# Kernel optimization log

Measured on AMD Instinct MI355X. Metric: run time of the kernel, lower is better.

## Reference

```python
import jax, jax.numpy as jnp
import numpy as np

B, N, IN_F, OUT_F = 32, 1024, 256, 256
ALPHA = 0.2  # LeakyReLU negative slope
NEG_INF = -9e15  # matches torch's -9000000000000000.0 masking constant


def setup_inputs() -> dict:
    key = jax.random.key(0)
    k1, k2, k3, k4 = jax.random.split(key, 4)
    h = jax.random.normal(k1, (B, N, IN_F), dtype=jnp.float32)
    adj = jax.random.randint(k2, (B, N, N), 0, 2, dtype=jnp.int32)
    W = jax.random.normal(k3, (OUT_F, IN_F), dtype=jnp.float32) * 0.05
    a = jax.random.normal(k4, (1, 2 * OUT_F), dtype=jnp.float32) * 0.05
    return {"h": h, "adj": adj, "W": W, "a": a}


def reference(h, adj, W, a):
    # Wh: (B, N, out)
    Wh = jnp.einsum("bni,oi->bno", h, W)
    # Decompose a([Wh_i || Wh_j]) = Wh_i . a1 + Wh_j . a2 (identical math,
    # avoids the O(B*N^2*2*out) concat intermediate of the torch code).
    a1 = a[0, :OUT_F]   # (out,)
    a2 = a[0, OUT_F:]   # (out,)
    si = Wh @ a1        # (B, N) score contribution of source node i
    sj = Wh @ a2        # (B, N) score contribution of neighbor node j
    e = jax.nn.leaky_relu(si[:, :, None] + sj[:, None, :], negative_slope=ALPHA)
    attention = jnp.where(adj > 0, e, NEG_INF)
    attention = jax.nn.softmax(attention, axis=-1)
    # dropout omitted (eval mode)
    h_prime = jnp.einsum("bij,bjo->bio", attention, Wh)
    return jax.nn.elu(h_prime)
```

## Files before the change

kernel.cpp:

```cpp
#include <hip/hip_runtime.h>
#include <hip/hip_bf16.h>


#define ALPHA 0.2f
#define LOG2E 1.44269504f

typedef __bf16 bf16x8 __attribute__((ext_vector_type(8)));
typedef __bf16 bf16x4 __attribute__((ext_vector_type(4)));
typedef float  f32x4  __attribute__((ext_vector_type(4)));
typedef unsigned long long u64;

__global__ __launch_bounds__(256) void k1_gemm1(const float* __restrict__ h,
                                                const float* __restrict__ W,
                                                const float* __restrict__ a_g,
                                                __bf16* __restrict__ whT,
                                                float* __restrict__ si,
                                                float* __restrict__ sj) {
    __shared__ __bf16 hA[64 * 72];
    __shared__ __bf16 hB[256 * 72];
    __shared__ float  red[512];
    const int t    = threadIdx.x;
    const int r0   = blockIdx.x * 64;
    const int b    = r0 >> 10;
    const int n0   = r0 & 1023;
    const int w    = t >> 6;
    const int l    = t & 63;
    const int ln   = l & 15;
    const int quad = l >> 4;

    f32x4 acc[4][4] = {};
    float4 ha_r[4], wb_r[16];

    #pragma unroll
    for (int it = 0; it < 4; ++it)
        ha_r[it] = *(const float4*)&h[(size_t)(r0 + it * 16 + (t >> 4)) * 256 + (t & 15) * 4];
    #pragma unroll
    for (int it = 0; it < 16; ++it)
        wb_r[it] = *(const float4*)&W[(size_t)(it * 16 + (t >> 4)) * 256 + (t & 15) * 4];

    for (int kc = 0; kc < 4; ++kc) {
        #pragma unroll
        for (int it = 0; it < 4; ++it) {
            const float4 v = ha_r[it];
            bf16x4 pv = {(__bf16)v.x, (__bf16)v.y, (__bf16)v.z, (__bf16)v.w};
            *(bf16x4*)&hA[(it * 16 + (t >> 4)) * 72 + (t & 15) * 4] = pv;
        }
        #pragma unroll
        for (int it = 0; it < 16; ++it) {
            const float4 v = wb_r[it];
            bf16x4 pv = {(__bf16)v.x, (__bf16)v.y, (__bf16)v.z, (__bf16)v.w};
            *(bf16x4*)&hB[(it * 16 + (t >> 4)) * 72 + (t & 15) * 4] = pv;
        }
        __syncthreads();
        if (kc < 3) {
            const int k0 = (kc + 1) * 64;
            #pragma unroll
            for (int it = 0; it < 4; ++it)
                ha_r[it] = *(const float4*)&h[(size_t)(r0 + it * 16 + (t >> 4)) * 256 + k0 + (t & 15) * 4];
            #pragma unroll
            for (int it = 0; it < 16; ++it)
                wb_r[it] = *(const float4*)&W[(size_t)(it * 16 + (t >> 4)) * 256 + k0 + (t & 15) * 4];
        }
        #pragma unroll
        for (int kk = 0; kk < 2; ++kk) {
            bf16x8 af[4], bfr[4];
            #pragma unroll
            for (int ri = 0; ri < 4; ++ri)
                af[ri] = *(const bf16x8*)&hA[(ri * 16 + ln) * 72 + kk * 32 + quad * 8];
            #pragma unroll
            for (int oi = 0; oi < 4; ++oi)
                bfr[oi] = *(const bf16x8*)&hB[(w * 64 + oi * 16 + ln) * 72 + kk * 32 + quad * 8];
            #pragma unroll
            for (int ri = 0; ri < 4; ++ri)
                #pragma unroll
                for (int oi = 0; oi < 4; ++oi)
                    acc[ri][oi] = __builtin_amdgcn_mfma_f32_16x16x32_bf16(
                        af[ri], bfr[oi], acc[ri][oi], 0, 0, 0);
        }
        __syncthreads();
    }

    #pragma unroll
    for (int ri = 0; ri < 4; ++ri) {
        const int n = ri * 16 + quad * 4;
        #pragma unroll
        for (int oi = 0; oi < 4; ++oi) {
            const int o = w * 64 + oi * 16 + ln;
            bf16x4 pv = {(__bf16)acc[ri][oi][0], (__bf16)acc[ri][oi][1],
                         (__bf16)acc[ri][oi][2], (__bf16)acc[ri][oi][3]};
            *(bf16x4*)&hB[o * 72 + n] = pv;
        }
    }
    __syncthreads();

    #pragma unroll
    for (int it = 0; it < 8; ++it) {
        const int o   = w * 64 + it * 8 + (l >> 3);
        const int seg = l & 7;
        const bf16x8 v = *(const bf16x8*)&hB[o * 72 + seg * 8];
        *(bf16x8*)&whT[((size_t)b * 256 + o) * 1024 + n0 + seg * 8] = v;
    }

    {
        float s1 = 0.f, s2 = 0.f;
        #pragma unroll 8
        for (int oi = 0; oi < 64; ++oi) {
            const int o = w * 64 + oi;
            const float v = (float)hB[o * 72 + l];
            s1 += v * a_g[o];
            s2 += v * a_g[256 + o];
        }
        red[w * 64 + l]       = s1;
        red[256 + w * 64 + l] = s2;
    }
    __syncthreads();
    if (t < 64) {
        si[b * 1024 + n0 + t] =
            (red[t] + red[64 + t] + red[128 + t] + red[192 + t]) * LOG2E;
    } else if (t < 128) {
        const int n = t - 64;
        sj[b * 1024 + n0 + n] =
            (red[256 + n] + red[320 + n] + red[384 + n] + red[448 + n]) * LOG2E;
    }
}

__global__ __launch_bounds__(256) void k3_attn(const int* __restrict__ adj,
                                               const __bf16* __restrict__ whT,
                                               const float* __restrict__ si_g,
                                               const float* __restrict__ sj_g,
                                               float* __restrict__ out) {
    __shared__ __bf16 lds_s[2][64 * 72];
    __shared__ float  lds_denom[64];
    const int t = threadIdx.x;
    const int orig = blockIdx.x;
    const int wgid = (orig & 7) * 64 + (orig >> 3);
    const int b    = wgid >> 4;
    const int i0   = (wgid & 15) << 6;
    const int w    = t >> 6;
    const int l    = t & 63;
    const int ln   = l & 15;
    const int quad = l >> 4;
    const int g    = t >> 4;
    const int j4   = t & 15;

    float si_r[4];
    #pragma unroll
    for (int m = 0; m < 4; ++m) si_r[m] = si_g[b * 1024 + i0 + m * 16 + g];

    float dsum[4] = {0.f, 0.f, 0.f, 0.f};
    f32x4 acc[4][4] = {};
    const __bf16* whTb = whT + (size_t)b * 256 * 1024;
    const int*    adjb = adj + ((size_t)(b * 1024 + i0)) * 1024;

    int4   amsk[4];
    float4 sjv;
    #pragma unroll
    for (int m = 0; m < 4; ++m)
        amsk[m] = *(const int4*)&adjb[(size_t)(m * 16 + g) * 1024 + j4 * 4];
    sjv = *(const float4*)&sj_g[b * 1024 + j4 * 4];

    #pragma unroll 2
    for (int jc = 0; jc < 16; ++jc) {
        const int j0 = jc * 64;
        __bf16* s_buf = (__bf16*)lds_s[jc & 1];

        bf16x8 bfr[2][4];
        #pragma unroll
        for (int kk = 0; kk < 2; ++kk)
            #pragma unroll
            for (int oi = 0; oi < 4; ++oi)
                bfr[kk][oi] = *(const bf16x8*)&whTb[
                    (size_t)(w * 64 + oi * 16 + ln) * 1024 + j0 + kk * 32 + quad * 8];

        #pragma unroll
        for (int m = 0; m < 4; ++m) {
            const int il = m * 16 + g;
            float e0 = si_r[m] + sjv.x; e0 = e0 > 0.f ? e0 : ALPHA * e0;
            float e1 = si_r[m] + sjv.y; e1 = e1 > 0.f ? e1 : ALPHA * e1;
            float e2 = si_r[m] + sjv.z; e2 = e2 > 0.f ? e2 : ALPHA * e2;
            float e3 = si_r[m] + sjv.w; e3 = e3 > 0.f ? e3 : ALPHA * e3;
            const float w0 = amsk[m].x > 0 ? exp2f(e0) : 0.f;
            const float w1 = amsk[m].y > 0 ? exp2f(e1) : 0.f;
            const float w2 = amsk[m].z > 0 ? exp2f(e2) : 0.f;
            const float w3 = amsk[m].w > 0 ? exp2f(e3) : 0.f;
            bf16x4 pv = {(__bf16)w0, (__bf16)w1, (__bf16)w2, (__bf16)w3};
            dsum[m] += (float)pv[0] + (float)pv[1] + (float)pv[2] + (float)pv[3];
            *(bf16x4*)&s_buf[il * 72 + j4 * 4] = pv;
        }

        if (jc < 15) {
            #pragma unroll
            for (int m = 0; m < 4; ++m)
                amsk[m] = *(const int4*)&adjb[(size_t)(m * 16 + g) * 1024 + j0 + 64 + j4 * 4];
            sjv = *(const float4*)&sj_g[b * 1024 + j0 + 64 + j4 * 4];
        }
        __syncthreads();

        #pragma unroll
        for (int kk = 0; kk < 2; ++kk) {
            bf16x8 af[4];
            #pragma unroll
            for (int ri = 0; ri < 4; ++ri)
                af[ri] = *(const bf16x8*)&s_buf[(ri * 16 + ln) * 72 + kk * 32 + quad * 8];
            #pragma unroll
            for (int ri = 0; ri < 4; ++ri)
                #pragma unroll
                for (int oi = 0; oi < 4; ++oi)
                    acc[ri][oi] = __builtin_amdgcn_mfma_f32_16x16x32_bf16(
                        af[ri], bfr[kk][oi], acc[ri][oi], 0, 0, 0);
        }
    }

    #pragma unroll
    for (int m = 0; m < 4; ++m) {
        float v = dsum[m];
        v += __shfl_xor(v, 1);
        v += __shfl_xor(v, 2);
        v += __shfl_xor(v, 4);
        v += __shfl_xor(v, 8);
        if (j4 == 0) lds_denom[m * 16 + g] = v;
    }
    __syncthreads();
    #pragma unroll
    for (int ri = 0; ri < 4; ++ri) {
        #pragma unroll
        for (int q = 0; q < 4; ++q) {
            const int il = ri * 16 + quad * 4 + q;
            const float dinv = 1.0f / fmaxf(lds_denom[il], 1e-30f);
            #pragma unroll
            for (int oi = 0; oi < 4; ++oi) {
                const int o = w * 64 + oi * 16 + ln;
                const float v = acc[ri][oi][q] * dinv;
                const float r = v > 0.f ? v : __expf(v) - 1.f;
                out[((size_t)(b * 1024 + i0 + il)) * 256 + o] = r;
            }
        }
    }
}

extern "C" void kernel_launch(void* const* d_in, const int* in_sizes, int n_in,
                              void* d_out, int out_size, void* d_ws, size_t ws_size,
                              hipStream_t stream) {
    const float* h   = (const float*)d_in[0];
    const int*   adj = (const int*)d_in[1];
    const float* W   = (const float*)d_in[2];
    const float* a   = (const float*)d_in[3];
    float* out = (float*)d_out;

    __bf16* whT = (__bf16*)d_ws;
    float*  si  = (float*)((char*)d_ws + (size_t)16777216);
    float*  sj  = (float*)((char*)d_ws + (size_t)16777216 + 131072);

    k1_gemm1<<<512, 256, 0, stream>>>(h, W, a, whT, si, sj);
    k3_attn<<<512, 256, 0, stream>>>(adj, whT, si, sj, out);
}
```

Before: 257.4 us.

## Halve attention tile rows, double grid, and explicitly double-buffer mask loads

Shrinks the attention kernel's row tile from 64 to 32 rows per block, doubling the grid to 1024 blocks, and sets launch bounds to request 4 blocks per SM for higher occupancy. The main loop is manually unrolled by two with ping-pong register buffers for the adjacency and sj prefetch, which are now issued earlier, before the exp computation. The intent is more waves to hide the latency of the adj stream and WhT loads. In exchange, each block re-reads the full WhT B operand, so that traffic doubles, and each MFMA B fragment is reused over fewer rows.

```diff
diff --git a/kernel.cpp b/kernel.cpp
--- a/kernel.cpp
+++ b/kernel.cpp
@@ -124,18 +124,72 @@
     }
 }
 
-__global__ __launch_bounds__(256) void k3_attn(const int* __restrict__ adj,
-                                               const __bf16* __restrict__ whT,
-                                               const float* __restrict__ si_g,
-                                               const float* __restrict__ sj_g,
-                                               float* __restrict__ out) {
-    __shared__ __bf16 lds_s[2][64 * 72];
-    __shared__ float  lds_denom[64];
+#define K3_BODY(JC, ACUR, SJCUR, ANXT, SJNXT, SBUF)                                    \
+  {                                                                                    \
+    const int j0 = (JC) * 64;                                                          \
+             \
+    bf16x8 bfr[2][4];                                                                  \
+    _Pragma("unroll")                                                                  \
+    for (int kk = 0; kk < 2; ++kk)                                                     \
+      _Pragma("unroll")                                                                \
+      for (int oi = 0; oi < 4; ++oi)                                                   \
+        bfr[kk][oi] = *(const bf16x8*)&whTb[                                           \
+            (size_t)(w * 64 + oi * 16 + ln) * 1024 + j0 + kk * 32 + quad * 8];         \
+            \
+    if ((JC) < 15) {                                                                   \
+      _Pragma("unroll")                                                                \
+      for (int m = 0; m < 2; ++m)                                                      \
+        ANXT[m] = *(const int4*)&adjb[(size_t)(m * 16 + g) * 1024 + j0 + 64 + j4 * 4]; \
+      SJNXT = *(const float4*)&sj_g[b * 1024 + j0 + 64 + j4 * 4];                      \
+    }                                                                                  \
+                \
+    _Pragma("unroll")                                                                  \
+    for (int m = 0; m < 2; ++m) {                                                      \
+      const int il = m * 16 + g;                                                       \
+      float e0 = si_r[m] + SJCUR.x; e0 = e0 > 0.f ? e0 : ALPHA * e0;                   \
+      float e1 = si_r[m] + SJCUR.y; e1 = e1 > 0.f ? e1 : ALPHA * e1;                   \
+      float e2 = si_r[m] + SJCUR.z; e2 = e2 > 0.f ? e2 : ALPHA * e2;                   \
+      float e3 = si_r[m] + SJCUR.w; e3 = e3 > 0.f ? e3 : ALPHA * e3;                   \
+      const float w0 = ACUR[m].x > 0 ? exp2f(e0) : 0.f;                                \
+      const float w1 = ACUR[m].y > 0 ? exp2f(e1) : 0.f;                                \
+      const float w2 = ACUR[m].z > 0 ? exp2f(e2) : 0.f;                                \
+      const float w3 = ACUR[m].w > 0 ? exp2f(e3) : 0.f;                                \
+      bf16x4 pv = {(__bf16)w0, (__bf16)w1, (__bf16)w2, (__bf16)w3};                    \
+      dsum[m] += (float)pv[0] + (float)pv[1] + (float)pv[2] + (float)pv[3];            \
+      *(bf16x4*)&SBUF[il * 72 + j4 * 4] = pv;                                          \
+    }                                                                                  \
+    __syncthreads();                                                                   \
+                         \
+    _Pragma("unroll")                                                                  \
+    for (int kk = 0; kk < 2; ++kk) {                                                   \
+      bf16x8 af[2];                                                                    \
+      _Pragma("unroll")                                                                \
+      for (int ri = 0; ri < 2; ++ri)                                                   \
+        af[ri] = *(const bf16x8*)&SBUF[(ri * 16 + ln) * 72 + kk * 32 + quad * 8];      \
+      _Pragma("unroll")                                                                \
+      for (int ri = 0; ri < 2; ++ri)                                                   \
+        _Pragma("unroll")                                                              \
+        for (int oi = 0; oi < 4; ++oi)                                                 \
+          acc[ri][oi] = __builtin_amdgcn_mfma_f32_16x16x32_bf16(                       \
+              af[ri], bfr[kk][oi], acc[ri][oi], 0, 0, 0);                              \
+    }                                                                                  \
+             \
+                                   \
+  }
+
+__global__ __launch_bounds__(256, 4) void k3_attn(const int* __restrict__ adj,
+                                                  const __bf16* __restrict__ whT,
+                                                  const float* __restrict__ si_g,
+                                                  const float* __restrict__ sj_g,
+                                                  float* __restrict__ out) {
+    __shared__ __bf16 lds_s0[32 * 72];
+    __shared__ __bf16 lds_s1[32 * 72];
+    __shared__ float  lds_denom[32];
     const int t = threadIdx.x;
     const int orig = blockIdx.x;
-    const int wgid = (orig & 7) * 64 + (orig >> 3);
-    const int b    = wgid >> 4;
-    const int i0   = (wgid & 15) << 6;
+    const int wgid = (orig & 7) * 128 + (orig >> 3);
+    const int b    = wgid >> 5;
+    const int i0   = (wgid & 31) << 5;
     const int w    = t >> 6;
     const int l    = t & 63;
     const int ln   = l & 15;
@@ -143,76 +197,29 @@
     const int g    = t >> 4;
     const int j4   = t & 15;
 
-    float si_r[4];
-    #pragma unroll
-    for (int m = 0; m < 4; ++m) si_r[m] = si_g[b * 1024 + i0 + m * 16 + g];
-
-    float dsum[4] = {0.f, 0.f, 0.f, 0.f};
-    f32x4 acc[4][4] = {};
+    float si_r[2];
+    #pragma unroll
+    for (int m = 0; m < 2; ++m) si_r[m] = si_g[b * 1024 + i0 + m * 16 + g];
+
+    float dsum[2] = {0.f, 0.f};
+    f32x4 acc[2][4] = {};
     const __bf16* whTb = whT + (size_t)b * 256 * 1024;
     const int*    adjb = adj + ((size_t)(b * 1024 + i0)) * 1024;
 
-    int4   amsk[4];
-    float4 sjv;
-    #pragma unroll
-    for (int m = 0; m < 4; ++m)
-        amsk[m] = *(const int4*)&adjb[(size_t)(m * 16 + g) * 1024 + j4 * 4];
-    sjv = *(const float4*)&sj_g[b * 1024 + j4 * 4];
-
-    #pragma unroll 2
-    for (int jc = 0; jc < 16; ++jc) {
-        const int j0 = jc * 64;
-        __bf16* s_buf = (__bf16*)lds_s[jc & 1];
-
-        bf16x8 bfr[2][4];
-        #pragma unroll
-        for (int kk = 0; kk < 2; ++kk)
-            #pragma unroll
-            for (int oi = 0; oi < 4; ++oi)
-                bfr[kk][oi] = *(const bf16x8*)&whTb[
-                    (size_t)(w * 64 + oi * 16 + ln) * 1024 + j0 + kk * 32 + quad * 8];
-
-        #pragma unroll
-        for (int m = 0; m < 4; ++m) {
-            const int il = m * 16 + g;
-            float e0 = si_r[m] + sjv.x; e0 = e0 > 0.f ? e0 : ALPHA * e0;
-            float e1 = si_r[m] + sjv.y; e1 = e1 > 0.f ? e1 : ALPHA * e1;
-            float e2 = si_r[m] + sjv.z; e2 = e2 > 0.f ? e2 : ALPHA * e2;
-            float e3 = si_r[m] + sjv.w; e3 = e3 > 0.f ? e3 : ALPHA * e3;
-            const float w0 = amsk[m].x > 0 ? exp2f(e0) : 0.f;
-            const float w1 = amsk[m].y > 0 ? exp2f(e1) : 0.f;
-            const float w2 = amsk[m].z > 0 ? exp2f(e2) : 0.f;
-            const float w3 = amsk[m].w > 0 ? exp2f(e3) : 0.f;
-            bf16x4 pv = {(__bf16)w0, (__bf16)w1, (__bf16)w2, (__bf16)w3};
-            dsum[m] += (float)pv[0] + (float)pv[1] + (float)pv[2] + (float)pv[3];
-            *(bf16x4*)&s_buf[il * 72 + j4 * 4] = pv;
-        }
-
-        if (jc < 15) {
-            #pragma unroll
-            for (int m = 0; m < 4; ++m)
-                amsk[m] = *(const int4*)&adjb[(size_t)(m * 16 + g) * 1024 + j0 + 64 + j4 * 4];
-            sjv = *(const float4*)&sj_g[b * 1024 + j0 + 64 + j4 * 4];
-        }
-        __syncthreads();
-
-        #pragma unroll
-        for (int kk = 0; kk < 2; ++kk) {
-            bf16x8 af[4];
-            #pragma unroll
-            for (int ri = 0; ri < 4; ++ri)
-                af[ri] = *(const bf16x8*)&s_buf[(ri * 16 + ln) * 72 + kk * 32 + quad * 8];
-            #pragma unroll
-            for (int ri = 0; ri < 4; ++ri)
-                #pragma unroll
-                for (int oi = 0; oi < 4; ++oi)
-                    acc[ri][oi] = __builtin_amdgcn_mfma_f32_16x16x32_bf16(
-                        af[ri], bfr[kk][oi], acc[ri][oi], 0, 0, 0);
-        }
-    }
-
-    #pragma unroll
-    for (int m = 0; m < 4; ++m) {
+    int4   a_c[2], a_n[2];
+    float4 sj_c, sj_n;
+    #pragma unroll
+    for (int m = 0; m < 2; ++m)
+        a_c[m] = *(const int4*)&adjb[(size_t)(m * 16 + g) * 1024 + j4 * 4];
+    sj_c = *(const float4*)&sj_g[b * 1024 + j4 * 4];
+
+    for (int jj = 0; jj < 8; ++jj) {
+        K3_BODY(2 * jj,     a_c, sj_c, a_n, sj_n, lds_s0);
+        K3_BODY(2 * jj + 1, a_n, sj_n, a_c, sj_c, lds_s1);
+    }
+
+    #pragma unroll
+    for (int m = 0; m < 2; ++m) {
         float v = dsum[m];
         v += __shfl_xor(v, 1);
         v += __shfl_xor(v, 2);
@@ -222,7 +229,7 @@
     }
     __syncthreads();
     #pragma unroll
-    for (int ri = 0; ri < 4; ++ri) {
+    for (int ri = 0; ri < 2; ++ri) {
         #pragma unroll
         for (int q = 0; q < 4; ++q) {
             const int il = ri * 16 + quad * 4 + q;
@@ -252,5 +259,5 @@
     float*  sj  = (float*)((char*)d_ws + (size_t)16777216 + 131072);
 
     k1_gemm1<<<512, 256, 0, stream>>>(h, W, a, whT, si, sj);
-    k3_attn<<<512, 256, 0, stream>>>(adj, whT, si, sj, out);
+    k3_attn<<<1024, 256, 0, stream>>>(adj, whT, si, sj, out);
 }
```

New measurement: 302.1 us. 1.17x slower.

## Compute attention weights directly in MFMA A-fragment registers, removing LDS staging

Applied to the files above, without the earlier changes.

The attention kernel now has each wave build its own bf16 probability fragments in registers, in the exact layout the MFMA A operand expects. This removes the shared-memory staging buffer and the per-chunk __syncthreads. Waves are regrouped as 2 row-halves by 2 output-column halves (32 rows by 128 columns each), the adjacency and sj loads are double-buffered by manual ping-pong, and MFMA issue priority is raised with s_setprio. The cost is that each row's exp2 work is now duplicated across the two column waves, whT fragment loads per wave double, and register pressure rises, with launch bounds requesting 2 blocks per CU.

```diff
diff --git a/kernel.cpp b/kernel.cpp
--- a/kernel.cpp
+++ b/kernel.cpp
@@ -124,116 +124,125 @@
     }
 }
 
-__global__ __launch_bounds__(256) void k3_attn(const int* __restrict__ adj,
-                                               const __bf16* __restrict__ whT,
-                                               const float* __restrict__ si_g,
-                                               const float* __restrict__ sj_g,
-                                               float* __restrict__ out) {
-    __shared__ __bf16 lds_s[2][64 * 72];
-    __shared__ float  lds_denom[64];
+
+#define SVAL(SI, SJE, AV) \
+    ({ float _e = (SI) + (SJE); _e = fmaxf(_e, ALPHA * _e); \
+       (AV) > 0 ? exp2f(_e) : 0.f; })
+
+#define K3_BODY(J, A0, A1, B0, B1, SJ0, SJ1, NA0, NA1, NB0, NB1, NSJ0, NSJ1)   \
+  {                                                                            \
+    const int j0 = (J) * 32;                                                   \
+        \
+              \
+                                                 \
+    bf16x8 bfr[8];                                                             \
+    _Pragma("unroll")                                                          \
+    for (int oi = 0; oi < 8; ++oi)                                             \
+      bfr[oi] = *(const bf16x8*)&whTb[                                         \
+          (size_t)(oc + oi * 16 + ln) * 1024 + j0 + quad * 8];                 \
+                               \
+    if ((J) < 31) {                                                            \
+      NA0 = *(const int4*)&adjw[(size_t)ln * 1024 + j0 + 32 + quad * 8];       \
+      NA1 = *(const int4*)&adjw[(size_t)ln * 1024 + j0 + 32 + quad * 8 + 4];   \
+      NB0 = *(const int4*)&adjw[(size_t)(ln + 16) * 1024 + j0 + 32 + quad * 8];\
+      NB1 = *(const int4*)&adjw[(size_t)(ln + 16) * 1024 + j0 + 32 + quad * 8 + 4]; \
+      NSJ0 = *(const float4*)&sj_g[bs + j0 + 32 + quad * 8];                   \
+      NSJ1 = *(const float4*)&sj_g[bs + j0 + 32 + quad * 8 + 4];               \
+    }                                                                          \
+      \
+    bf16x8 af0, af1;                                                           \
+    af0[0] = (__bf16)SVAL(si0, SJ0.x, A0.x);                                   \
+    af0[1] = (__bf16)SVAL(si0, SJ0.y, A0.y);                                   \
+    af0[2] = (__bf16)SVAL(si0, SJ0.z, A0.z);                                   \
+    af0[3] = (__bf16)SVAL(si0, SJ0.w, A0.w);                                   \
+    af0[4] = (__bf16)SVAL(si0, SJ1.x, A1.x);                                   \
+    af0[5] = (__bf16)SVAL(si0, SJ1.y, A1.y);                                   \
+    af0[6] = (__bf16)SVAL(si0, SJ1.z, A1.z);                                   \
+    af0[7] = (__bf16)SVAL(si0, SJ1.w, A1.w);                                   \
+    af1[0] = (__bf16)SVAL(si1, SJ0.x, B0.x);                                   \
+    af1[1] = (__bf16)SVAL(si1, SJ0.y, B0.y);                                   \
+    af1[2] = (__bf16)SVAL(si1, SJ0.z, B0.z);                                   \
+    af1[3] = (__bf16)SVAL(si1, SJ0.w, B0.w);                                   \
+    af1[4] = (__bf16)SVAL(si1, SJ1.x, B1.x);                                   \
+    af1[5] = (__bf16)SVAL(si1, SJ1.y, B1.y);                                   \
+    af1[6] = (__bf16)SVAL(si1, SJ1.z, B1.z);                                   \
+    af1[7] = (__bf16)SVAL(si1, SJ1.w, B1.w);                                   \
+    dsum0 += (float)af0[0] + (float)af0[1] + (float)af0[2] + (float)af0[3]     \
+           + (float)af0[4] + (float)af0[5] + (float)af0[6] + (float)af0[7];    \
+    dsum1 += (float)af1[0] + (float)af1[1] + (float)af1[2] + (float)af1[3]     \
+           + (float)af1[4] + (float)af1[5] + (float)af1[6] + (float)af1[7];    \
+                                                \
+    __builtin_amdgcn_s_setprio(1);                                             \
+    _Pragma("unroll")                                                          \
+    for (int oi = 0; oi < 8; ++oi) {                                           \
+      acc0[oi] = __builtin_amdgcn_mfma_f32_16x16x32_bf16(af0, bfr[oi],         \
+                                                         acc0[oi], 0, 0, 0);   \
+      acc1[oi] = __builtin_amdgcn_mfma_f32_16x16x32_bf16(af1, bfr[oi],         \
+                                                         acc1[oi], 0, 0, 0);   \
+    }                                                                          \
+    __builtin_amdgcn_s_setprio(0);                                             \
+  }
+
+__global__ __launch_bounds__(256, 2) void k3_attn(const int* __restrict__ adj,
+                                                  const __bf16* __restrict__ whT,
+                                                  const float* __restrict__ si_g,
+                                                  const float* __restrict__ sj_g,
+                                                  float* __restrict__ out) {
     const int t = threadIdx.x;
     const int orig = blockIdx.x;
     const int wgid = (orig & 7) * 64 + (orig >> 3);
     const int b    = wgid >> 4;
     const int i0   = (wgid & 15) << 6;
     const int w    = t >> 6;
+    const int wr   = w >> 1;
+    const int oc   = (w & 1) * 128;
     const int l    = t & 63;
     const int ln   = l & 15;
     const int quad = l >> 4;
-    const int g    = t >> 4;
-    const int j4   = t & 15;
-
-    float si_r[4];
-    #pragma unroll
-    for (int m = 0; m < 4; ++m) si_r[m] = si_g[b * 1024 + i0 + m * 16 + g];
-
-    float dsum[4] = {0.f, 0.f, 0.f, 0.f};
-    f32x4 acc[4][4] = {};
+    const int bs   = b * 1024;
+
     const __bf16* whTb = whT + (size_t)b * 256 * 1024;
-    const int*    adjb = adj + ((size_t)(b * 1024 + i0)) * 1024;
-
-    int4   amsk[4];
-    float4 sjv;
-    #pragma unroll
-    for (int m = 0; m < 4; ++m)
-        amsk[m] = *(const int4*)&adjb[(size_t)(m * 16 + g) * 1024 + j4 * 4];
-    sjv = *(const float4*)&sj_g[b * 1024 + j4 * 4];
-
-    #pragma unroll 2
-    for (int jc = 0; jc < 16; ++jc) {
-        const int j0 = jc * 64;
-        __bf16* s_buf = (__bf16*)lds_s[jc & 1];
-
-        bf16x8 bfr[2][4];
-        #pragma unroll
-        for (int kk = 0; kk < 2; ++kk)
-            #pragma unroll
-            for (int oi = 0; oi < 4; ++oi)
-                bfr[kk][oi] = *(const bf16x8*)&whTb[
-                    (size_t)(w * 64 + oi * 16 + ln) * 1024 + j0 + kk * 32 + quad * 8];
-
-        #pragma unroll
-        for (int m = 0; m < 4; ++m) {
-            const int il = m * 16 + g;
-            float e0 = si_r[m] + sjv.x; e0 = e0 > 0.f ? e0 : ALPHA * e0;
-            float e1 = si_r[m] + sjv.y; e1 = e1 > 0.f ? e1 : ALPHA * e1;
-            float e2 = si_r[m] + sjv.z; e2 = e2 > 0.f ? e2 : ALPHA * e2;
-            float e3 = si_r[m] + sjv.w; e3 = e3 > 0.f ? e3 : ALPHA * e3;
-            const float w0 = amsk[m].x > 0 ? exp2f(e0) : 0.f;
-            const float w1 = amsk[m].y > 0 ? exp2f(e1) : 0.f;
-            const float w2 = amsk[m].z > 0 ? exp2f(e2) : 0.f;
-            const float w3 = amsk[m].w > 0 ? exp2f(e3) : 0.f;
-            bf16x4 pv = {(__bf16)w0, (__bf16)w1, (__bf16)w2, (__bf16)w3};
-            dsum[m] += (float)pv[0] + (float)pv[1] + (float)pv[2] + (float)pv[3];
-            *(bf16x4*)&s_buf[il * 72 + j4 * 4] = pv;
-        }
-
-        if (jc < 15) {
-            #pragma unroll
-            for (int m = 0; m < 4; ++m)
-                amsk[m] = *(const int4*)&adjb[(size_t)(m * 16 + g) * 1024 + j0 + 64 + j4 * 4];
-            sjv = *(const float4*)&sj_g[b * 1024 + j0 + 64 + j4 * 4];
-        }
-        __syncthreads();
-
-        #pragma unroll
-        for (int kk = 0; kk < 2; ++kk) {
-            bf16x8 af[4];
-            #pragma unroll
-            for (int ri = 0; ri < 4; ++ri)
-                af[ri] = *(const bf16x8*)&s_buf[(ri * 16 + ln) * 72 + kk * 32 + quad * 8];
-            #pragma unroll
-            for (int ri = 0; ri < 4; ++ri)
-                #pragma unroll
-                for (int oi = 0; oi < 4; ++oi)
-                    acc[ri][oi] = __builtin_amdgcn_mfma_f32_16x16x32_bf16(
-                        af[ri], bfr[kk][oi], acc[ri][oi], 0, 0, 0);
-        }
-    }
-
-    #pragma unroll
-    for (int m = 0; m < 4; ++m) {
-        float v = dsum[m];
-        v += __shfl_xor(v, 1);
-        v += __shfl_xor(v, 2);
-        v += __shfl_xor(v, 4);
-        v += __shfl_xor(v, 8);
-        if (j4 == 0) lds_denom[m * 16 + g] = v;
-    }
-    __syncthreads();
-    #pragma unroll
-    for (int ri = 0; ri < 4; ++ri) {
-        #pragma unroll
-        for (int q = 0; q < 4; ++q) {
-            const int il = ri * 16 + quad * 4 + q;
-            const float dinv = 1.0f / fmaxf(lds_denom[il], 1e-30f);
-            #pragma unroll
-            for (int oi = 0; oi < 4; ++oi) {
-                const int o = w * 64 + oi * 16 + ln;
-                const float v = acc[ri][oi][q] * dinv;
-                const float r = v > 0.f ? v : __expf(v) - 1.f;
-                out[((size_t)(b * 1024 + i0 + il)) * 256 + o] = r;
-            }
+    const int*    adjw = adj + ((size_t)(bs + i0 + wr * 32)) * 1024;
+
+    const float si0 = si_g[bs + i0 + wr * 32 + ln];
+    const float si1 = si_g[bs + i0 + wr * 32 + 16 + ln];
+
+    float dsum0 = 0.f, dsum1 = 0.f;
+    f32x4 acc0[8] = {}, acc1[8] = {};
+
+    int4   a0_c, a1_c, b0_c, b1_c, a0_n, a1_n, b0_n, b1_n;
+    float4 sj0_c, sj1_c, sj0_n, sj1_n;
+    a0_c  = *(const int4*)&adjw[(size_t)ln * 1024 + quad * 8];
+    a1_c  = *(const int4*)&adjw[(size_t)ln * 1024 + quad * 8 + 4];
+    b0_c  = *(const int4*)&adjw[(size_t)(ln + 16) * 1024 + quad * 8];
+    b1_c  = *(const int4*)&adjw[(size_t)(ln + 16) * 1024 + quad * 8 + 4];
+    sj0_c = *(const float4*)&sj_g[bs + quad * 8];
+    sj1_c = *(const float4*)&sj_g[bs + quad * 8 + 4];
+
+    for (int jj = 0; jj < 16; ++jj) {
+        K3_BODY(2 * jj,     a0_c, a1_c, b0_c, b1_c, sj0_c, sj1_c,
+                            a0_n, a1_n, b0_n, b1_n, sj0_n, sj1_n);
+        K3_BODY(2 * jj + 1, a0_n, a1_n, b0_n, b1_n, sj0_n, sj1_n,
+                            a0_c, a1_c, b0_c, b1_c, sj0_c, sj1_c);
+    }
+
+    float d0 = dsum0; d0 += __shfl_xor(d0, 16); d0 += __shfl_xor(d0, 32);
+    float d1 = dsum1; d1 += __shfl_xor(d1, 16); d1 += __shfl_xor(d1, 32);
+
+    const int rbase = bs + i0 + wr * 32;
+    #pragma unroll
+    for (int q = 0; q < 4; ++q) {
+        const int   rloc = quad * 4 + q;
+        const float inv0 = 1.0f / fmaxf(__shfl(d0, rloc), 1e-30f);
+        const float inv1 = 1.0f / fmaxf(__shfl(d1, rloc), 1e-30f);
+        #pragma unroll
+        for (int oi = 0; oi < 8; ++oi) {
+            float v0 = acc0[oi][q] * inv0;
+            v0 = v0 > 0.f ? v0 : __expf(v0) - 1.f;
+            out[(size_t)(rbase + rloc) * 256 + oc + oi * 16 + ln] = v0;
+            float v1 = acc1[oi][q] * inv1;
+            v1 = v1 > 0.f ? v1 : __expf(v1) - 1.f;
+            out[(size_t)(rbase + 16 + rloc) * 256 + oc + oi * 16 + ln] = v1;
         }
     }
 }
```

Result: slower. 303.7 us (+18.0%).

## Pack adjacency into bitmasks and stage Wh tiles through LDS in attention kernel

Applied to the files above, without the earlier changes.

Adds a pre-pass kernel that ballots the int32 adjacency into 64-bit bitmasks laid out per (batch, j-chunk, row), so the attention kernel reads compact masks instead of the full int adjacency. The attention kernel now cooperatively loads the Wh^T tile into LDS with register prefetch of the next chunk, uses a manually double-unrolled loop with explicit barriers and setprio around the MFMA block, and declares an occupancy hint of two blocks per SM. The extra pass still reads the whole adjacency once, so the net saving depends on how much the attention kernel's adjacency reads were exposed rather than hidden. The single LDS staging buffer also needs two barriers per chunk.

```diff
diff --git a/kernel.cpp b/kernel.cpp
--- a/kernel.cpp
+++ b/kernel.cpp
@@ -9,6 +9,23 @@
 typedef __bf16 bf16x4 __attribute__((ext_vector_type(4)));
 typedef float  f32x4  __attribute__((ext_vector_type(4)));
 typedef unsigned long long u64;
+
+__global__ __launch_bounds__(256) void k0_mask(const int* __restrict__ adj,
+                                               u64* __restrict__ maskT) {
+    const int wid = (blockIdx.x * 256 + threadIdx.x) >> 6;
+    const int l   = threadIdx.x & 63;
+    const size_t base = (size_t)wid * 64;
+    #pragma unroll 4
+    for (int it = 0; it < 64; ++it) {
+        const size_t word = base + it;
+        const int b  = (int)(word >> 14);
+        const int jc = (int)((word >> 10) & 15);
+        const int i  = (int)(word & 1023);
+        const int v  = adj[(((size_t)b << 10) + i) * 1024 + jc * 64 + l];
+        const u64 m  = __ballot(v > 0);
+        if (l == 0) maskT[word] = m;
+    }
+}
 
 __global__ __launch_bounds__(256) void k1_gemm1(const float* __restrict__ h,
                                                 const float* __restrict__ W,
@@ -124,12 +141,76 @@
     }
 }
 
-__global__ __launch_bounds__(256) void k3_attn(const int* __restrict__ adj,
-                                               const __bf16* __restrict__ whT,
-                                               const float* __restrict__ si_g,
-                                               const float* __restrict__ sj_g,
-                                               float* __restrict__ out) {
-    __shared__ __bf16 lds_s[2][64 * 72];
+#define K3_BODY(JC, MC, SJC, MN, SJN)                                          \
+  {                                                                            \
+    const int j0 = (JC) * 64;                                                  \
+     \
+    _Pragma("unroll")                                                          \
+    for (int it = 0; it < 8; ++it)                                             \
+      *(bf16x8*)&lds_w[(it * 32 + (t >> 3)) * 72 + (t & 7) * 8] = vreg[it];    \
+              \
+    if ((JC) < 15) {                                                           \
+      _Pragma("unroll")                                                        \
+      for (int it = 0; it < 8; ++it)                                           \
+        vreg[it] = *(const bf16x8*)&whTb[                                      \
+            (size_t)(it * 32 + (t >> 3)) * 1024 + j0 + 64 + (t & 7) * 8];      \
+      _Pragma("unroll")                                                        \
+      for (int m = 0; m < 4; ++m)                                              \
+        MN[m] = maskTb[(size_t)((JC) + 1) * 1024 + i0 + m * 16 + g];           \
+      SJN = *(const float4*)&sj_g[bs + j0 + 64 + j4 * 4];                      \
+    }                                                                          \
+         \
+    _Pragma("unroll")                                                          \
+    for (int m = 0; m < 4; ++m) {                                              \
+      const int il = m * 16 + g;                                               \
+      const unsigned bits = (unsigned)(MC[m] >> (4 * j4)) & 0xFu;              \
+      float e0 = si_r[m] + SJC.x; e0 = fmaxf(e0, ALPHA * e0);                  \
+      float e1 = si_r[m] + SJC.y; e1 = fmaxf(e1, ALPHA * e1);                  \
+      float e2 = si_r[m] + SJC.z; e2 = fmaxf(e2, ALPHA * e2);                  \
+      float e3 = si_r[m] + SJC.w; e3 = fmaxf(e3, ALPHA * e3);                  \
+      const float w0 = (bits & 1u) ? exp2f(e0) : 0.f;                          \
+      const float w1 = (bits & 2u) ? exp2f(e1) : 0.f;                          \
+      const float w2 = (bits & 4u) ? exp2f(e2) : 0.f;                          \
+      const float w3 = (bits & 8u) ? exp2f(e3) : 0.f;                          \
+      bf16x4 pv = {(__bf16)w0, (__bf16)w1, (__bf16)w2, (__bf16)w3};            \
+      dsum[m] += (float)pv[0] + (float)pv[1] + (float)pv[2] + (float)pv[3];    \
+      *(bf16x4*)&lds_s[il * 72 + j4 * 4] = pv;                                 \
+    }                                                                          \
+                       \
+    asm volatile("s_waitcnt lgkmcnt(0)");                                      \
+    __builtin_amdgcn_s_barrier();                                              \
+                                                    \
+    __builtin_amdgcn_s_setprio(1);                                             \
+    _Pragma("unroll")                                                          \
+    for (int kk = 0; kk < 2; ++kk) {                                           \
+      bf16x8 af[4], bfr[4];                                                    \
+      _Pragma("unroll")                                                        \
+      for (int ri = 0; ri < 4; ++ri)                                           \
+        af[ri] = *(const bf16x8*)&lds_s[(ri * 16 + ln) * 72 + kk * 32 + quad * 8]; \
+      _Pragma("unroll")                                                        \
+      for (int oi = 0; oi < 4; ++oi)                                           \
+        bfr[oi] = *(const bf16x8*)&lds_w[(w * 64 + oi * 16 + ln) * 72 + kk * 32 + quad * 8]; \
+      _Pragma("unroll")                                                        \
+      for (int ri = 0; ri < 4; ++ri)                                           \
+        _Pragma("unroll")                                                      \
+        for (int oi = 0; oi < 4; ++oi)                                         \
+          acc[ri][oi] = __builtin_amdgcn_mfma_f32_16x16x32_bf16(               \
+              af[ri], bfr[oi], acc[ri][oi], 0, 0, 0);                          \
+    }                                                                          \
+    __builtin_amdgcn_s_setprio(0);                                             \
+     \
+                                \
+    asm volatile("s_waitcnt lgkmcnt(0)");                                      \
+    __builtin_amdgcn_s_barrier();                                              \
+  }
+
+__global__ __launch_bounds__(256, 2) void k3_attn(const u64* __restrict__ maskT,
+                                                  const __bf16* __restrict__ whT,
+                                                  const float* __restrict__ si_g,
+                                                  const float* __restrict__ sj_g,
+                                                  float* __restrict__ out) {
+    __shared__ __bf16 lds_w[256 * 72];
+    __shared__ __bf16 lds_s[64 * 72];
     __shared__ float  lds_denom[64];
     const int t = threadIdx.x;
     const int orig = blockIdx.x;
@@ -142,73 +223,31 @@
     const int quad = l >> 4;
     const int g    = t >> 4;
     const int j4   = t & 15;
+    const int bs   = b * 1024;
 
     float si_r[4];
     #pragma unroll
-    for (int m = 0; m < 4; ++m) si_r[m] = si_g[b * 1024 + i0 + m * 16 + g];
+    for (int m = 0; m < 4; ++m) si_r[m] = si_g[bs + i0 + m * 16 + g];
 
     float dsum[4] = {0.f, 0.f, 0.f, 0.f};
     f32x4 acc[4][4] = {};
-    const __bf16* whTb = whT + (size_t)b * 256 * 1024;
-    const int*    adjb = adj + ((size_t)(b * 1024 + i0)) * 1024;
-
-    int4   amsk[4];
-    float4 sjv;
-    #pragma unroll
-    for (int m = 0; m < 4; ++m)
-        amsk[m] = *(const int4*)&adjb[(size_t)(m * 16 + g) * 1024 + j4 * 4];
-    sjv = *(const float4*)&sj_g[b * 1024 + j4 * 4];
-
-    #pragma unroll 2
-    for (int jc = 0; jc < 16; ++jc) {
-        const int j0 = jc * 64;
-        __bf16* s_buf = (__bf16*)lds_s[jc & 1];
-
-        bf16x8 bfr[2][4];
-        #pragma unroll
-        for (int kk = 0; kk < 2; ++kk)
-            #pragma unroll
-            for (int oi = 0; oi < 4; ++oi)
-                bfr[kk][oi] = *(const bf16x8*)&whTb[
-                    (size_t)(w * 64 + oi * 16 + ln) * 1024 + j0 + kk * 32 + quad * 8];
-
-        #pragma unroll
-        for (int m = 0; m < 4; ++m) {
-            const int il = m * 16 + g;
-            float e0 = si_r[m] + sjv.x; e0 = e0 > 0.f ? e0 : ALPHA * e0;
-            float e1 = si_r[m] + sjv.y; e1 = e1 > 0.f ? e1 : ALPHA * e1;
-            float e2 = si_r[m] + sjv.z; e2 = e2 > 0.f ? e2 : ALPHA * e2;
-            float e3 = si_r[m] + sjv.w; e3 = e3 > 0.f ? e3 : ALPHA * e3;
-            const float w0 = amsk[m].x > 0 ? exp2f(e0) : 0.f;
-            const float w1 = amsk[m].y > 0 ? exp2f(e1) : 0.f;
-            const float w2 = amsk[m].z > 0 ? exp2f(e2) : 0.f;
-            const float w3 = amsk[m].w > 0 ? exp2f(e3) : 0.f;
-            bf16x4 pv = {(__bf16)w0, (__bf16)w1, (__bf16)w2, (__bf16)w3};
-            dsum[m] += (float)pv[0] + (float)pv[1] + (float)pv[2] + (float)pv[3];
-            *(bf16x4*)&s_buf[il * 72 + j4 * 4] = pv;
-        }
-
-        if (jc < 15) {
-            #pragma unroll
-            for (int m = 0; m < 4; ++m)
-                amsk[m] = *(const int4*)&adjb[(size_t)(m * 16 + g) * 1024 + j0 + 64 + j4 * 4];
-            sjv = *(const float4*)&sj_g[b * 1024 + j0 + 64 + j4 * 4];
-        }
-        __syncthreads();
-
-        #pragma unroll
-        for (int kk = 0; kk < 2; ++kk) {
-            bf16x8 af[4];
-            #pragma unroll
-            for (int ri = 0; ri < 4; ++ri)
-                af[ri] = *(const bf16x8*)&s_buf[(ri * 16 + ln) * 72 + kk * 32 + quad * 8];
-            #pragma unroll
-            for (int ri = 0; ri < 4; ++ri)
-                #pragma unroll
-                for (int oi = 0; oi < 4; ++oi)
-                    acc[ri][oi] = __builtin_amdgcn_mfma_f32_16x16x32_bf16(
-                        af[ri], bfr[kk][oi], acc[ri][oi], 0, 0, 0);
-        }
+    const __bf16* whTb   = whT + (size_t)b * 256 * 1024;
+    const u64*    maskTb = maskT + (size_t)b * 16384;
+
+    bf16x8 vreg[8];
+    u64    m_c[4], m_n[4];
+    float4 sj_c, sj_n;
+
+    #pragma unroll
+    for (int it = 0; it < 8; ++it)
+        vreg[it] = *(const bf16x8*)&whTb[(size_t)(it * 32 + (t >> 3)) * 1024 + (t & 7) * 8];
+    #pragma unroll
+    for (int m = 0; m < 4; ++m) m_c[m] = maskTb[i0 + m * 16 + g];
+    sj_c = *(const float4*)&sj_g[bs + j4 * 4];
+
+    for (int jj = 0; jj < 8; ++jj) {
+        K3_BODY(2 * jj,     m_c, sj_c, m_n, sj_n);
+        K3_BODY(2 * jj + 1, m_n, sj_n, m_c, sj_c);
     }
 
     #pragma unroll
@@ -232,7 +271,7 @@
                 const int o = w * 64 + oi * 16 + ln;
                 const float v = acc[ri][oi][q] * dinv;
                 const float r = v > 0.f ? v : __expf(v) - 1.f;
-                out[((size_t)(b * 1024 + i0 + il)) * 256 + o] = r;
+                out[((size_t)(bs + i0 + il)) * 256 + o] = r;
             }
         }
     }
@@ -247,10 +286,12 @@
     const float* a   = (const float*)d_in[3];
     float* out = (float*)d_out;
 
-    __bf16* whT = (__bf16*)d_ws;
-    float*  si  = (float*)((char*)d_ws + (size_t)16777216);
-    float*  sj  = (float*)((char*)d_ws + (size_t)16777216 + 131072);
-
+    __bf16* whT   = (__bf16*)d_ws;
+    float*  si    = (float*)((char*)d_ws + (size_t)16777216);
+    float*  sj    = (float*)((char*)d_ws + (size_t)16777216 + 131072);
+    u64*    maskT = (u64*)((char*)d_ws + (size_t)16777216 + 262144);
+
+    k0_mask<<<2048, 256, 0, stream>>>(adj, maskT);
     k1_gemm1<<<512, 256, 0, stream>>>(h, W, a, whT, si, sj);
-    k3_attn<<<512, 256, 0, stream>>>(adj, whT, si, sj, out);
-}
+    k3_attn<<<512, 256, 0, stream>>>(maskT, whT, si, sj, out);
+}
```

New measurement: 285.0 us. 1.11x slower.
